# Kernel optimization log

Measured on AMD Instinct MI355X. Metric: run time of the kernel, lower is better.

Reference implementation:

```python
import jax, jax.numpy as jnp
import numpy as np
import math
from jax import lax

# cfg['MODEL'] constants
MU = 0.1          # FISTA step size
LMBD = 0.1        # LAMBDA[0], sparsity weight
N_DICT = 1        # EXPANSION_FACTOR
N_STEPS = 6       # NUM_LAYERS (FISTA iterations)
K = 3             # kernel_size
PAD = 1           # padding
STRIDE = 1        # stride (POOLING=False, stride passed to conv)
DN = ('NCHW', 'OIHW', 'NCHW')


def _conv(x, w):
    # F.conv2d(x, w, stride=1, padding=PAD)
    return lax.conv_general_dilated(x, w, (STRIDE, STRIDE), [(PAD, PAD), (PAD, PAD)], dimension_numbers=DN)


def _conv_t(y, w):
    # F.conv_transpose2d(y, w, stride=1, padding=PAD) == conv2d with flipped, in/out-swapped kernel, pad K-1-PAD
    wt = jnp.transpose(jnp.flip(w, (-1, -2)), (1, 0, 2, 3))  # [Cin, Cout, K, K]
    p = K - 1 - PAD
    return lax.conv_general_dilated(y, wt, (1, 1), [(p, p), (p, p)], dimension_numbers=DN)


def _shrink(z, thr):
    # non_negative=True soft-threshold: relu(z - thr)
    return jax.nn.relu(z - thr)


def setup_inputs() -> dict:
    key = jax.random.key(0)
    k1, k2 = jax.random.split(key)
    x = jax.random.normal(k1, (16, 64, 56, 56), dtype=jnp.float32)
    # dictionary weight [out_channels, in_channels*n_dict, K, K], kaiming-ish scale
    W = jax.random.normal(k2, (128, 64 * N_DICT, K, K), dtype=jnp.float32) * 0.05
    return {"x": x, "W": W}


def reference(x, W):
    # w_norm: each output filter normalized to unit Frobenius norm
    Wn = W / jnp.sqrt(jnp.sum(W * W, axis=(1, 2, 3), keepdims=True) + 1e-12)
    thr = MU * LMBD
    xr = jnp.tile(x, (1, N_DICT, 1, 1)) if N_DICT > 1 else x

    # FISTA iteration 0: c = shrink(mu * D^T x)
    c = _shrink(MU * _conv(xr, Wn), thr)
    y = c
    c_prev = c
    t = 1.0
    for _ in range(N_STEPS - 1):
        r = xr - _conv_t(y, Wn)                       # residual x - D c
        c_new = _shrink(y + MU * _conv(r, Wn), thr)   # gradient step + shrink
        t_next = (1.0 + math.sqrt(1.0 + 4.0 * t * t)) / 2.0
        y = c_new + ((t - 1.0) / t_next) * (c_new - c_prev)  # momentum
        c_prev = c_new
        t = t_next
    # POOLING=False -> DictConv2d returns the sparse code directly
    return c_prev
```

## Files before the change

### kernel.cpp

```cpp
#include <hip/hip_runtime.h>
#include <hip/hip_bf16.h>
#include <math.h>

typedef __attribute__((ext_vector_type(8))) short short8;
typedef __attribute__((ext_vector_type(16))) float f32x16;

#define MU_  0.1f
#define THR_ 0.01f

static __device__ inline short f2bf(float f) {
    __hip_bfloat16 h = __float2bfloat16(f);
    return *reinterpret_cast<short*>(&h);
}
static __device__ inline float bf2f(unsigned short u) {
    unsigned int x = ((unsigned int)u) << 16;
    return __builtin_bit_cast(float, x);
}

__global__ __launch_bounds__(256) void zero_kernel(float4* p, int n4) {
    int i = blockIdx.x * 256 + threadIdx.x;
    if (i < n4) p[i] = make_float4(0.f, 0.f, 0.f, 0.f);
}

__global__ __launch_bounds__(64) void wnorm_pack(
    const float* __restrict__ W, short* __restrict__ Wf, short* __restrict__ Wt) {
    int co = blockIdx.x, ci = threadIdx.x;
    const float* wp = W + (co * 64 + ci) * 9;
    float v[9]; float s = 0.f;
#pragma unroll
    for (int t = 0; t < 9; ++t) { v[t] = wp[t]; s += v[t] * v[t]; }
#pragma unroll
    for (int off = 32; off; off >>= 1) s += __shfl_xor(s, off, 64);
    float inv = 1.0f / sqrtf(s + 1e-12f);
#pragma unroll
    for (int t = 0; t < 9; ++t) {
        Wf[(t * 128 + co) * 64 + (ci ^ ((co & 7) << 3))] = f2bf(v[t] * inv);
        Wt[(t * 64 + ci) * 128 + (co ^ ((ci & 7) << 3))] = f2bf(v[8 - t] * inv);
    }
}

__global__ __launch_bounds__(256) void pack_x(
    const float* __restrict__ x, short* __restrict__ Xp) {
    __shared__ float lx[64 * 57];
    int row = blockIdx.x, n = blockIdx.y, tid = threadIdx.x;
    short* dst = Xp + ((size_t)(n * 58 + row) * 68) * 64;
    if (row >= 1 && row <= 56) {
        int h = row - 1;
        for (int j = tid; j < 64 * 56; j += 256) {
            int ci = j / 56, w = j - ci * 56;
            lx[ci * 57 + w] = x[((size_t)(n * 64 + ci)) * 3136 + h * 56 + w];
        }
        __syncthreads();
        for (int j = tid; j < 68 * 64; j += 256) {
            int s = j >> 6, ci = j & 63;
            float val = (s >= 2 && s < 58) ? lx[ci * 57 + (s - 2)] : 0.f;
            dst[(s << 6) + (ci ^ ((s & 7) << 3))] = f2bf(val);
        }
    } else {
        for (int j = tid; j < 68 * 64; j += 256) dst[j] = 0;
    }
}

__global__ __launch_bounds__(256) void conv_fwd(
    const short* __restrict__ inp,
    const short* __restrict__ Wf,
    float* __restrict__ y,
    unsigned short* __restrict__ cpb,
    short* __restrict__ Yp,
    float* __restrict__ outp, int mode, float beta) {
    __shared__ short xs[3 * 68 * 64];
    const int r = blockIdx.x + 1, cb = blockIdx.y, n = blockIdx.z, tid = threadIdx.x;
    {
        const short8* src = (const short8*)(inp + ((size_t)(n * 58 + (r - 1)) * 68) * 64);
        short8* d = (short8*)xs;
        for (int j = tid; j < 1632; j += 256) d[j] = src[j];
    }
    __syncthreads();

    const int lane = tid & 63, wid = tid >> 6, qh = lane >> 5, v0 = lane & 31;
    const int ms = wid & 1, ph = wid >> 1;
    const int co = cb * 64 + ms * 32 + v0;
    const int v  = ph * 32 + v0;
    const int h  = r - 1;
    const bool valid = v < 56;
    const size_t obase = ((size_t)(n * 128 + cb * 64 + ms * 32)) * 3136 +
                         (size_t)h * 56 + v;

    float ypre[16]; unsigned short cpre[16];
    if (mode != 0 && valid) {
#pragma unroll
        for (int reg = 0; reg < 16; ++reg) {
            const int crl = (reg & 3) + 8 * (reg >> 2) + 4 * qh;
            ypre[reg] = y[obase + (size_t)crl * 3136];
            if (mode == 1) cpre[reg] = cpb[obase + (size_t)crl * 3136];
        }
    }

    int goffA[4], bg[3][4];
#pragma unroll
    for (int s = 0; s < 4; ++s) goffA[s] = 8 * ((2 * s + qh) ^ (v0 & 7));
#pragma unroll
    for (int dw = 0; dw < 3; ++dw) {
        int key = (v0 + dw + 1) & 7;
#pragma unroll
        for (int s = 0; s < 4; ++s) bg[dw][s] = 8 * ((2 * s + qh) ^ key);
    }
    const short* wbase = Wf + co * 64;

    f32x16 acc;
#pragma unroll
    for (int i = 0; i < 16; ++i) acc[i] = 0.f;

    short8 Af[2][4];
#pragma unroll
    for (int s = 0; s < 4; ++s) Af[0][s] = *(const short8*)(wbase + goffA[s]);

#pragma unroll
    for (int t = 0; t < 9; ++t) {
        if (t + 1 < 9) {
#pragma unroll
            for (int s = 0; s < 4; ++s)
                Af[(t + 1) & 1][s] = *(const short8*)(wbase + (t + 1) * 8192 + goffA[s]);
        }
        const int dh = t / 3, dw = t % 3;
        const int b_base = (dh * 68 + (v + dw + 1)) * 64;
#pragma unroll
        for (int s = 0; s < 4; ++s) {
            short8 bv = *(const short8*)(xs + b_base + bg[dw][s]);
            acc = __builtin_amdgcn_mfma_f32_32x32x16_bf16(Af[t & 1][s], bv, acc, 0, 0, 0);
        }
    }

    __syncthreads();
    short* tb = xs;
#pragma unroll
    for (int reg = 0; reg < 16; ++reg) {
        const int crl = (reg & 3) + 8 * (reg >> 2) + 4 * qh;
        const size_t o = obase + (size_t)crl * 3136;
        const float a = acc[reg];
        float ynew = 0.f;
        if (mode == 0) {
            float c = fmaxf(MU_ * a - THR_, 0.f);
            ynew = c;
            if (valid) { y[o] = c; cpb[o] = (unsigned short)f2bf(c); }
        } else if (mode == 1) {
            if (valid) {
                float c = fmaxf(ypre[reg] + MU_ * a - THR_, 0.f);
                ynew = c + beta * (c - bf2f(cpre[reg]));
                y[o] = ynew; cpb[o] = (unsigned short)f2bf(c);
            }
        } else {
            if (valid) {
                float c = fmaxf(ypre[reg] + MU_ * a - THR_, 0.f);
                outp[o] = c;
            }
        }
        if (mode != 2) tb[v * 72 + ms * 32 + crl] = f2bf(ynew);
    }
    if (mode != 2) {
        __syncthreads();
        short* ydst = Yp + ((size_t)(n * 58 + r) * 68) * 128;
        for (int item = tid; item < 56 * 8; item += 256) {
            int vv = item >> 3, g = item & 7;
            short8 val = *(const short8*)(tb + vv * 72 + 8 * g);
            int s = vv + 2;
            *(short8*)(ydst + s * 128 + 8 * ((g + 8 * cb) ^ (s & 7))) = val;
        }
    }
}

__global__ __launch_bounds__(256) void conv_t(
    const short* __restrict__ Ypb,
    const short* __restrict__ Wt,
    const float* __restrict__ x,
    short* __restrict__ Rp) {
    __shared__ short ys[3 * 68 * 128];
    const int r = blockIdx.x + 1, n = blockIdx.y, tid = threadIdx.x;
    {
        const short8* src = (const short8*)(Ypb + ((size_t)(n * 58 + (r - 1)) * 68) * 128);
        short8* d = (short8*)ys;
        for (int j = tid; j < 3264; j += 256) d[j] = src[j];
    }
    __syncthreads();

    const int lane = tid & 63, wid = tid >> 6, qh = lane >> 5, l31 = lane & 31;
    const int cib = (wid & 1) * 32, vb = (wid >> 1) * 32;
    const int ci = cib + l31;
    const int v = vb + l31;
    const int h = r - 1;
    const bool valid = v < 56;

    const size_t xbase = ((size_t)n * 64) * 3136 + (size_t)h * 56 + v;
    float xpre[16];
    if (valid) {
#pragma unroll
        for (int reg = 0; reg < 16; ++reg) {
            const int cir = cib + (reg & 3) + 8 * (reg >> 2) + 4 * qh;
            xpre[reg] = x[xbase + (size_t)cir * 3136];
        }
    }

    int goffA[8], bg[3][8];
#pragma unroll
    for (int s = 0; s < 8; ++s) goffA[s] = 8 * ((2 * s + qh) ^ (ci & 7));
#pragma unroll
    for (int dw = 0; dw < 3; ++dw) {
        int key = (l31 + dw + 1) & 7;
#pragma unroll
        for (int s = 0; s < 8; ++s) bg[dw][s] = 8 * ((2 * s + qh) ^ key);
    }
    const short* wbase = Wt + ci * 128;

    f32x16 acc;
#pragma unroll
    for (int i = 0; i < 16; ++i) acc[i] = 0.f;

    short8 Af[2][8];
#pragma unroll
    for (int s = 0; s < 8; ++s) Af[0][s] = *(const short8*)(wbase + goffA[s]);

#pragma unroll
    for (int t = 0; t < 9; ++t) {
        if (t + 1 < 9) {
#pragma unroll
            for (int s = 0; s < 8; ++s)
                Af[(t + 1) & 1][s] = *(const short8*)(wbase + (t + 1) * 8192 + goffA[s]);
        }
        const int dh = t / 3, dw = t % 3;
        const int b_base = (dh * 68 + (v + dw + 1)) * 128;
#pragma unroll
        for (int s = 0; s < 8; ++s) {
            short8 bv = *(const short8*)(ys + b_base + bg[dw][s]);
            acc = __builtin_amdgcn_mfma_f32_32x32x16_bf16(Af[t & 1][s], bv, acc, 0, 0, 0);
        }
    }

    __syncthreads();
    short* tb = ys;
#pragma unroll
    for (int reg = 0; reg < 16; ++reg) {
        const int cir = cib + (reg & 3) + 8 * (reg >> 2) + 4 * qh;
        float rv = 0.f;
        if (valid) rv = xpre[reg] - acc[reg];
        tb[v * 72 + cir] = f2bf(rv);
    }
    __syncthreads();
    short* rdst = Rp + ((size_t)(n * 58 + r) * 68) * 64;
    for (int item = tid; item < 56 * 8; item += 256) {
        int vv = item >> 3, g = item & 7;
        short8 val = *(const short8*)(tb + vv * 72 + 8 * g);
        int s = vv + 2;
        *(short8*)(rdst + (s << 6) + 8 * (g ^ (s & 7))) = val;
    }
}

extern "C" void kernel_launch(void* const* d_in, const int* in_sizes, int n_in,
                              void* d_out, int out_size, void* d_ws, size_t ws_size,
                              hipStream_t stream) {
    const float* x = (const float*)d_in[0];
    const float* W = (const float*)d_in[1];
    float* out = (float*)d_out;

    const size_t YN = 6422528;
    const size_t XPN = (size_t)16 * 58 * 68 * 64;
    const size_t YPN = (size_t)16 * 58 * 68 * 128;
    float* y  = (float*)d_ws;
    unsigned short* cpb = (unsigned short*)(y + YN);
    short* Xp = (short*)(cpb + YN);
    short* Rp = Xp + XPN;
    short* Yp = Rp + XPN;
    short* Wf = Yp + YPN;
    short* Wt = Wf + 9 * 128 * 64;

    const int n4 = (int)((XPN + YPN) * 2 / 16);
    hipLaunchKernelGGL(zero_kernel, dim3((n4 + 255) / 256), dim3(256), 0, stream,
                       (float4*)Rp, n4);
    hipLaunchKernelGGL(wnorm_pack, dim3(128), dim3(64), 0, stream, W, Wf, Wt);
    hipLaunchKernelGGL(pack_x, dim3(58, 16), dim3(256), 0, stream, x, Xp);

    dim3 gf(56, 2, 16), gt(56, 16), b(256, 1, 1);
    hipLaunchKernelGGL(conv_fwd, gf, b, 0, stream, Xp, Wf, y, cpb, Yp,
                       (float*)nullptr, 0, 0.f);
    double t = 1.0;
    for (int it = 1; it <= 5; ++it) {
        hipLaunchKernelGGL(conv_t, gt, b, 0, stream, Yp, Wt, x, Rp);
        double tn = (1.0 + sqrt(1.0 + 4.0 * t * t)) / 2.0;
        float beta = (float)((t - 1.0) / tn);
        hipLaunchKernelGGL(conv_fwd, gf, b, 0, stream, Rp, Wf, y, cpb, Yp,
                           (it == 5) ? out : (float*)nullptr, (it == 5) ? 2 : 1,
                           beta);
        t = tn;
    }
}
```

Baseline: 428.1 us.

## Keep FISTA state in padded bf16 layout and read x from packed buffer

Drops the fp32 NCHW y buffer and the strided per-register reads of y, c_prev and x. Those state values now live in the padded channel-last bf16 buffers (Yp, plus a new Cp), which are loaded as coalesced short8 vectors and staged through swizzled shared memory. Residuals in conv_t also read the bf16 packed Xp instead of fp32 x. This cuts global traffic and removes uncoalesced accesses, but the momentum state y is now kept in bf16 rather than fp32, which lowers precision. Cp sits in the workspace right after Yp, so the zero pass over Rp and Yp does not clear it.

```diff
diff --git a/kernel.cpp b/kernel.cpp
--- a/kernel.cpp
+++ b/kernel.cpp
@@ -64,9 +64,8 @@
 __global__ __launch_bounds__(256) void conv_fwd(
     const short* __restrict__ inp,
     const short* __restrict__ Wf,
-    float* __restrict__ y,
-    unsigned short* __restrict__ cpb,
     short* __restrict__ Yp,
+    short* __restrict__ Cp,
     float* __restrict__ outp, int mode, float beta) {
     __shared__ short xs[3 * 68 * 64];
     const int r = blockIdx.x + 1, cb = blockIdx.y, n = blockIdx.z, tid = threadIdx.x;
@@ -75,6 +74,22 @@
         short8* d = (short8*)xs;
         for (int j = tid; j < 1632; j += 256) d[j] = src[j];
     }
+
+    const size_t prow = ((size_t)(n * 58 + r) * 68) * 128;
+    short8 yold8[2], cold8[2];
+    int pvv[2], pg[2]; bool pok[2];
+#pragma unroll
+    for (int k = 0; k < 2; ++k) {
+        int item = tid + k * 256;
+        pok[k] = item < 448;
+        pvv[k] = item >> 3; pg[k] = item & 7;
+        if (mode != 0 && pok[k]) {
+            int s = pvv[k] + 2;
+            size_t off = prow + (size_t)s * 128 + 8 * ((pg[k] + 8 * cb) ^ (s & 7));
+            yold8[k] = *(const short8*)(Yp + off);
+            if (mode == 1) cold8[k] = *(const short8*)(Cp + off);
+        }
+    }
     __syncthreads();
 
     const int lane = tid & 63, wid = tid >> 6, qh = lane >> 5, v0 = lane & 31;
@@ -82,19 +97,6 @@
     const int co = cb * 64 + ms * 32 + v0;
     const int v  = ph * 32 + v0;
     const int h  = r - 1;
-    const bool valid = v < 56;
-    const size_t obase = ((size_t)(n * 128 + cb * 64 + ms * 32)) * 3136 +
-                         (size_t)h * 56 + v;
-
-    float ypre[16]; unsigned short cpre[16];
-    if (mode != 0 && valid) {
-#pragma unroll
-        for (int reg = 0; reg < 16; ++reg) {
-            const int crl = (reg & 3) + 8 * (reg >> 2) + 4 * qh;
-            ypre[reg] = y[obase + (size_t)crl * 3136];
-            if (mode == 1) cpre[reg] = cpb[obase + (size_t)crl * 3136];
-        }
-    }
 
     int goffA[4], bg[3][4];
 #pragma unroll
@@ -132,39 +134,56 @@
     }
 
     __syncthreads();
-    short* tb = xs;
+    short* tb_y = xs;
+    short* tb_c = xs + 4608;
+    if (mode != 0) {
+#pragma unroll
+        for (int k = 0; k < 2; ++k) if (pok[k]) {
+            int o = pvv[k] * 72 + 8 * (pg[k] ^ (pvv[k] & 3));
+            *(short8*)(tb_y + o) = yold8[k];
+            if (mode == 1) *(short8*)(tb_c + o) = cold8[k];
+        }
+    }
+    __syncthreads();
 #pragma unroll
     for (int reg = 0; reg < 16; ++reg) {
         const int crl = (reg & 3) + 8 * (reg >> 2) + 4 * qh;
-        const size_t o = obase + (size_t)crl * 3136;
+        const int lch = ms * 32 + crl;
+        const int slot = v * 72 + (lch ^ ((v & 3) << 3));
         const float a = acc[reg];
-        float ynew = 0.f;
         if (mode == 0) {
             float c = fmaxf(MU_ * a - THR_, 0.f);
-            ynew = c;
-            if (valid) { y[o] = c; cpb[o] = (unsigned short)f2bf(c); }
+            short cb16 = f2bf(c);
+            tb_y[slot] = cb16;
+            tb_c[slot] = cb16;
         } else if (mode == 1) {
-            if (valid) {
-                float c = fmaxf(ypre[reg] + MU_ * a - THR_, 0.f);
-                ynew = c + beta * (c - bf2f(cpre[reg]));
-                y[o] = ynew; cpb[o] = (unsigned short)f2bf(c);
+            float yold = bf2f((unsigned short)tb_y[slot]);
+            float cold = bf2f((unsigned short)tb_c[slot]);
+            float c = fmaxf(yold + MU_ * a - THR_, 0.f);
+            float ynew = c + beta * (c - cold);
+            tb_y[slot] = f2bf(ynew);
+            tb_c[slot] = f2bf(c);
+        } else {
+            if (v < 56) {
+                float yold = bf2f((unsigned short)tb_y[slot]);
+                float c = fmaxf(yold + MU_ * a - THR_, 0.f);
+                outp[((size_t)(n * 128 + cb * 64 + lch)) * 3136 + h * 56 + v] = c;
             }
-        } else {
-            if (valid) {
-                float c = fmaxf(ypre[reg] + MU_ * a - THR_, 0.f);
-                outp[o] = c;
-            }
-        }
-        if (mode != 2) tb[v * 72 + ms * 32 + crl] = f2bf(ynew);
+        }
     }
     if (mode != 2) {
         __syncthreads();
-        short* ydst = Yp + ((size_t)(n * 58 + r) * 68) * 128;
-        for (int item = tid; item < 56 * 8; item += 256) {
+        short* ydst = Yp + prow;
+        short* cdst = Cp + prow;
+        for (int item = tid; item < 448; item += 256) {
             int vv = item >> 3, g = item & 7;
-            short8 val = *(const short8*)(tb + vv * 72 + 8 * g);
+            int so = vv * 72 + 8 * (g ^ (vv & 3));
+            short8 yv = *(const short8*)(tb_y + so);
+            short8 cv = *(const short8*)(tb_c + so);
             int s = vv + 2;
-            *(short8*)(ydst + s * 128 + 8 * ((g + 8 * cb) ^ (s & 7))) = val;
+            size_t off = (size_t)s * 128 + 8 * ((g + 8 * cb) ^ (s & 7));
+            *(short8*)(ydst + off) = yv;
+            *(short8*)(cdst + off) = cv;
         }
     }
 }
@@ -172,7 +191,7 @@
 __global__ __launch_bounds__(256) void conv_t(
     const short* __restrict__ Ypb,
     const short* __restrict__ Wt,
-    const float* __restrict__ x,
+    const short* __restrict__ Xp,
     short* __restrict__ Rp) {
     __shared__ short ys[3 * 68 * 128];
     const int r = blockIdx.x + 1, n = blockIdx.y, tid = threadIdx.x;
@@ -181,24 +200,26 @@
         short8* d = (short8*)ys;
         for (int j = tid; j < 3264; j += 256) d[j] = src[j];
     }
+
+    const size_t prow = ((size_t)(n * 58 + r) * 68) * 64;
+    short8 xold8[2];
+    int pvv[2], pg[2]; bool pok[2];
+#pragma unroll
+    for (int k = 0; k < 2; ++k) {
+        int item = tid + k * 256;
+        pok[k] = item < 448;
+        pvv[k] = item >> 3; pg[k] = item & 7;
+        if (pok[k]) {
+            int s = pvv[k] + 2;
+            xold8[k] = *(const short8*)(Xp + prow + (size_t)s * 64 + 8 * (pg[k] ^ (s & 7)));
+        }
+    }
     __syncthreads();
 
     const int lane = tid & 63, wid = tid >> 6, qh = lane >> 5, l31 = lane & 31;
     const int cib = (wid & 1) * 32, vb = (wid >> 1) * 32;
     const int ci = cib + l31;
     const int v = vb + l31;
-    const int h = r - 1;
-    const bool valid = v < 56;
-
-    const size_t xbase = ((size_t)n * 64) * 3136 + (size_t)h * 56 + v;
-    float xpre[16];
-    if (valid) {
-#pragma unroll
-        for (int reg = 0; reg < 16; ++reg) {
-            const int cir = cib + (reg & 3) + 8 * (reg >> 2) + 4 * qh;
-            xpre[reg] = x[xbase + (size_t)cir * 3136];
-        }
-    }
 
     int goffA[8], bg[3][8];
 #pragma unroll
@@ -238,19 +259,24 @@
     __syncthreads();
     short* tb = ys;
 #pragma unroll
+    for (int k = 0; k < 2; ++k) if (pok[k]) {
+        *(short8*)(tb + pvv[k] * 72 + 8 * (pg[k] ^ (pvv[k] & 3))) = xold8[k];
+    }
+    __syncthreads();
+#pragma unroll
     for (int reg = 0; reg < 16; ++reg) {
         const int cir = cib + (reg & 3) + 8 * (reg >> 2) + 4 * qh;
-        float rv = 0.f;
-        if (valid) rv = xpre[reg] - acc[reg];
-        tb[v * 72 + cir] = f2bf(rv);
-    }
-    __syncthreads();
-    short* rdst = Rp + ((size_t)(n * 58 + r) * 68) * 64;
-    for (int item = tid; item < 56 * 8; item += 256) {
+        const int slot = v * 72 + (cir ^ ((v & 3) << 3));
+        float xo = bf2f((unsigned short)tb[slot]);
+        tb[slot] = f2bf(xo - acc[reg]);
+    }
+    __syncthreads();
+    short* rdst = Rp + prow;
+    for (int item = tid; item < 448; item += 256) {
         int vv = item >> 3, g = item & 7;
-        short8 val = *(const short8*)(tb + vv * 72 + 8 * g);
+        short8 val = *(const short8*)(tb + vv * 72 + 8 * (g ^ (vv & 3)));
         int s = vv + 2;
-        *(short8*)(rdst + (s << 6) + 8 * (g ^ (s & 7))) = val;
+        *(short8*)(rdst + (size_t)s * 64 + 8 * (g ^ (s & 7))) = val;
     }
 }
 
@@ -261,15 +287,13 @@
     const float* W = (const float*)d_in[1];
     float* out = (float*)d_out;
 
-    const size_t YN = 6422528;
     const size_t XPN = (size_t)16 * 58 * 68 * 64;
-    const size_t YPN = (size_t)16 * 58 * 68 * 128;
-    float* y  = (float*)d_ws;
-    unsigned short* cpb = (unsigned short*)(y + YN);
-    short* Xp = (short*)(cpb + YN);
+    const size_t YPN = 2 * XPN;
+    short* Xp = (short*)d_ws;
     short* Rp = Xp + XPN;
     short* Yp = Rp + XPN;
-    short* Wf = Yp + YPN;
+    short* Cp = Yp + YPN;
+    short* Wf = Cp + YPN;
     short* Wt = Wf + 9 * 128 * 64;
 
     const int n4 = (int)((XPN + YPN) * 2 / 16);
@@ -279,14 +303,14 @@
     hipLaunchKernelGGL(pack_x, dim3(58, 16), dim3(256), 0, stream, x, Xp);
 
     dim3 gf(56, 2, 16), gt(56, 16), b(256, 1, 1);
-    hipLaunchKernelGGL(conv_fwd, gf, b, 0, stream, Xp, Wf, y, cpb, Yp,
+    hipLaunchKernelGGL(conv_fwd, gf, b, 0, stream, Xp, Wf, Yp, Cp,
                        (float*)nullptr, 0, 0.f);
     double t = 1.0;
     for (int it = 1; it <= 5; ++it) {
-        hipLaunchKernelGGL(conv_t, gt, b, 0, stream, Yp, Wt, x, Rp);
+        hipLaunchKernelGGL(conv_t, gt, b, 0, stream, Yp, Wt, Xp, Rp);
         double tn = (1.0 + sqrt(1.0 + 4.0 * t * t)) / 2.0;
         float beta = (float)((t - 1.0) / tn);
-        hipLaunchKernelGGL(conv_fwd, gf, b, 0, stream, Rp, Wf, y, cpb, Yp,
+        hipLaunchKernelGGL(conv_fwd, gf, b, 0, stream, Rp, Wf, Yp, Cp,
                            (it == 5) ? out : (float*)nullptr, (it == 5) ? 2 : 1,
                            beta);
         t = tn;
```

After: 406.1 us. -5.1%, faster.
